# Performance work log

Hardware: AMD Instinct MI355X
Metric: run time of the kernel (lower is better)

## Reference

```python
import jax, jax.numpy as jnp
import numpy as np

H = 64          # hiddenNum
C3 = 3 * H      # 192 attention channels
FL = 7          # filterLen
PAD = FL // 2
NORM = 1.0 / np.sqrt(C3).astype(np.float32)


def _u(key, shape, stdv):
    return jax.random.uniform(key, shape, jnp.float32, -stdv, stdv)


def setup_inputs() -> dict:
    key = jax.random.key(0)
    ks = iter(jax.random.split(key, 64))
    B, N = 16, 1024
    x = jax.random.normal(next(ks), (B, N, 128), jnp.float32)
    adj = jax.random.uniform(next(ks), (B, N, N), jnp.float32)
    degree = jax.random.uniform(next(ks), (B, N, N), jnp.float32)
    eps = jax.random.normal(next(ks), (B, C3), jnp.float32) * 0.1
    d = {"x": x, "adj": adj, "degree": degree, "eps": eps}
    # GCN params (torch uniform(-1/sqrt(out), 1/sqrt(out)))
    for name, fi, fo in [("gcn1", 128, 2 * H), ("gcn2", H, 4 * H), ("gcn3", 2 * H, 6 * H)]:
        s = 1.0 / np.sqrt(fo)
        d[name + "_w"] = _u(next(ks), (fi, fo), s)
        d[name + "_b"] = _u(next(ks), (fo,), s)
    # Conv1d params [out, in, k]
    for name, ci, co in [("conv1", 128, 2 * H), ("conv2", H, 4 * H), ("conv3", 2 * H, 6 * H)]:
        s = 1.0 / np.sqrt(ci * FL)
        d[name + "_w"] = _u(next(ks), (co, ci, FL), s)
        d[name + "_b"] = _u(next(ks), (co,), s)
    # 1x1 conv Q/K/V projections
    s = 1.0 / np.sqrt(C3)
    for name in ["srq", "srk", "srv", "drq", "drk", "drv"]:
        d[name + "_w"] = _u(next(ks), (C3, C3, 1), s)
        d[name + "_b"] = _u(next(ks), (C3,), s)
    # Linear layers [out, in]
    for name in ["l1", "l2"]:
        d[name + "_w"] = _u(next(ks), (C3, C3), s)
        d[name + "_b"] = _u(next(ks), (C3,), s)
    return d


def _glu_last(y):
    o, g = jnp.split(y, 2, axis=-1)
    return o * jax.nn.sigmoid(g)


def _glu_ch(y):
    o, g = jnp.split(y, 2, axis=1)
    return o * jax.nn.sigmoid(g)


def _conv1d(x, w, b, pad):
    y = jax.lax.conv_general_dilated(x, w, (1,), [(pad, pad)],
                                     dimension_numbers=("NCH", "OIH", "NCH"))
    return y + b[None, :, None]


def reference(x, adj, degree, eps,
              gcn1_w, gcn1_b, gcn2_w, gcn2_b, gcn3_w, gcn3_b,
              conv1_w, conv1_b, conv2_w, conv2_b, conv3_w, conv3_b,
              srq_w, srq_b, srk_w, srk_b, srv_w, srv_b,
              drq_w, drq_b, drk_w, drk_b, drv_w, drv_b,
              l1_w, l1_b, l2_w, l2_b):
    # normalized adjacency: D @ A @ D  (batched dense bmm, as in the original)
    adj_n = jnp.matmul(jnp.matmul(degree, adj), degree)  # [B,N,N]

    def gcn(inp, W, b):
        return jnp.matmul(adj_n, inp @ W) + b

    # GCN branch with GLU gating (eval mode: dropout = identity)
    g1 = _glu_last(gcn(x, gcn1_w, gcn1_b))      # [B,N,H]
    g2 = _glu_last(gcn(g1, gcn2_w, gcn2_b))     # [B,N,2H]
    g3 = _glu_last(gcn(g2, gcn3_w, gcn3_b))     # [B,N,3H]
    gcn_out = jnp.transpose(g3, (0, 2, 1))      # [B,3H,N]

    # CNN branch with gated convs
    xc = jnp.transpose(x, (0, 2, 1))            # [B,128,N]
    c1 = _glu_ch(_conv1d(xc, conv1_w, conv1_b, PAD))   # [B,H,N]
    c2 = _glu_ch(_conv1d(c1, conv2_w, conv2_b, PAD))   # [B,2H,N]
    cnn_out = _glu_ch(_conv1d(c2, conv3_w, conv3_b, PAD))  # [B,3H,N]

    # 1x1-conv Q/K/V projections
    def p1x1(t, w, b):
        return jnp.einsum('oc,bcn->bon', w[:, :, 0], t) + b[None, :, None]

    SRQ = p1x1(cnn_out, srq_w, srq_b)
    SRK = p1x1(cnn_out, srk_w, srk_b)
    SRV = p1x1(cnn_out, srv_w, srv_b)
    DRQ = p1x1(gcn_out, drq_w, drq_b)
    DRK = p1x1(gcn_out, drk_w, drk_b)
    DRV = p1x1(gcn_out, drv_w, drv_b)

    # dual cross-attention; NOTE: scale applied AFTER softmax, as in the source
    attSR = jax.nn.softmax(jnp.einsum('bcn,bcm->bnm', SRQ, DRK), axis=-1) * NORM
    outSR = jnp.einsum('bnm,bcm->bnc', attSR, SRV)   # [B,N,3H]
    attDR = jax.nn.softmax(jnp.einsum('bcn,bcm->bnm', DRQ, SRK), axis=-1) * NORM
    outDR = jnp.einsum('bnm,bcm->bnc', attDR, DRV)   # [B,N,3H]

    feat = outSR + outDR                              # [B,N,3H]
    pooled = jnp.mean(feat, axis=1)                   # AdaptiveAvgPool1d(1) over N -> [B,3H]

    out1 = jax.nn.relu(pooled @ l1_w.T + l1_b)        # mean
    out2 = jax.nn.relu(pooled @ l2_w.T + l2_b)        # logvar
    std = jnp.exp(0.5 * out2)
    out0 = eps * std + out1                           # reparametrize
    return (out0, out1, out2)
```

## Files before the change

### kernel.cpp

```cpp
#include <hip/hip_runtime.h>


#define Bn 16
#define Nn 1024
#define C3n 192
static __device__ __constant__ float NORM_C = 0.07216878364870322f;

typedef short bf16x8 __attribute__((ext_vector_type(8)));
typedef float f32x4 __attribute__((ext_vector_type(4)));
typedef unsigned short u16;
typedef unsigned short u16x4 __attribute__((ext_vector_type(4)));

__device__ __forceinline__ u16 bf16rn(float x)
{
  unsigned b = __float_as_uint(x);
  b += 0x7fffu + ((b >> 16) & 1u);
  return (u16)(b >> 16);
}
__device__ __forceinline__ float fromh(u16 h) { return __uint_as_float(((unsigned)h) << 16); }

template<int TM, int TN, bool OUTB, int BIAS, bool ACC, bool OUTT>
__global__ __launch_bounds__(256, 2) void mgemm_k(
    const u16* __restrict__ A, long sA, int lda,
    const u16* __restrict__ B, long sB, int ldb,
    const float* __restrict__ bias,
    float* __restrict__ Cf, u16* __restrict__ Cb,
    int M, int N, int K)
{
  constexpr int WMN = (TM >= 128) ? 2 : 1;
  constexpr int WNN = 4 / WMN;
  constexpr int WTM = TM / WMN, WTN = TN / WNN;
  constexpr int FM = WTM / 16, FN = WTN / 16;
  constexpr int BBASE = TM * 128;
  __shared__ __align__(16) char sm[(TM + TN) * 128];

  const int bz = (int)blockIdx.z;
  const int n0 = blockIdx.x * TN, m0 = blockIdx.y * TM;
  const int tid = threadIdx.x, lane = tid & 63, w = tid >> 6;
  const int wm0 = (w / WNN) * WTM, wn0 = (w % WNN) * WTN;

  bf16x8 rA[TM / 32], rB[TN / 32];
  auto loadA = [&](int k0) {
    const u16* p = A + bz * sA + (long)m0 * lda + k0;
#pragma unroll
    for (int i = 0; i < TM / 32; ++i) {
      const int v = tid + i * 256, row = v >> 3, vc = v & 7;
      rA[i] = *(const bf16x8*)(p + (long)row * lda + vc * 8);
    }
  };
  auto storeA = [&]() {
#pragma unroll
    for (int i = 0; i < TM / 32; ++i) {
      const int v = tid + i * 256, row = v >> 3, vc = v & 7;
      *(bf16x8*)(sm + row * 128 + ((vc * 16) ^ ((row & 7) << 4))) = rA[i];
    }
  };
  auto loadB = [&](int k0) {
    const u16* p = B + bz * sB + (long)n0 * ldb + k0;
#pragma unroll
    for (int i = 0; i < TN / 32; ++i) {
      const int v = tid + i * 256, row = v >> 3, vc = v & 7;
      rB[i] = *(const bf16x8*)(p + (long)row * ldb + vc * 8);
    }
  };
  auto storeB = [&]() {
#pragma unroll
    for (int i = 0; i < TN / 32; ++i) {
      const int v = tid + i * 256, row = v >> 3, vc = v & 7;
      *(bf16x8*)(sm + BBASE + row * 128 + ((vc * 16) ^ ((row & 7) << 4))) = rB[i];
    }
  };

  f32x4 acc[FM][FN];
#pragma unroll
  for (int c = 0; c < FM; ++c)
#pragma unroll
    for (int d = 0; d < FN; ++d) acc[c][d] = (f32x4)(0.0f);

  loadA(0); loadB(0);
  for (int k0 = 0; k0 < K; k0 += 64) {
    storeA(); storeB();
    __syncthreads();
    if (k0 + 64 < K) { loadA(k0 + 64); loadB(k0 + 64); }
#pragma unroll
    for (int s = 0; s < 2; ++s) {
      const int kb = s * 64 + ((lane >> 4) << 4);
      bf16x8 ah[FM], bh[FN];
#pragma unroll
      for (int c = 0; c < FM; ++c) {
        const int ar = wm0 + c * 16 + (lane & 15);
        ah[c] = *(const bf16x8*)(sm + ar * 128 + (kb ^ ((ar & 7) << 4)));
      }
#pragma unroll
      for (int d = 0; d < FN; ++d) {
        const int br = wn0 + d * 16 + (lane & 15);
        bh[d] = *(const bf16x8*)(sm + BBASE + br * 128 + (kb ^ ((br & 7) << 4)));
      }
#pragma unroll
      for (int c = 0; c < FM; ++c)
#pragma unroll
        for (int d = 0; d < FN; ++d)
          acc[c][d] = __builtin_amdgcn_mfma_f32_16x16x32_bf16(ah[c], bh[d], acc[c][d], 0, 0, 0);
    }
    __syncthreads();
  }

  const long cb = (long)bz * M * N;
#pragma unroll
  for (int c = 0; c < FM; ++c)
#pragma unroll
    for (int d = 0; d < FN; ++d) {
      const int row0 = m0 + wm0 + c * 16 + (lane >> 4) * 4;
      const int col = n0 + wn0 + d * 16 + (lane & 15);
      if constexpr (OUTT) {
        u16x4 vv;
#pragma unroll
        for (int r = 0; r < 4; ++r) vv[r] = bf16rn(acc[c][d][r]);
        *(u16x4*)(Cb + cb + (long)col * M + row0) = vv;
      } else {
        float bcol = 0.f;
        if constexpr (BIAS == 1) bcol = bias[col];
#pragma unroll
        for (int r = 0; r < 4; ++r) {
          const int row = row0 + r;
          float v = acc[c][d][r];
          if constexpr (BIAS == 1) v += bcol;
          if constexpr (BIAS == 2) v += bias[row];
          const long idx = cb + (long)row * N + col;
          if constexpr (OUTB) {
            Cb[idx] = bf16rn(v);
          } else {
            if constexpr (ACC) v += Cf[idx];
            Cf[idx] = v;
          }
        }
      }
    }
}

__device__ __forceinline__ void gemm64_body(char* sm,
    const u16* __restrict__ A, int lda, const u16* __restrict__ B, int ldb,
    const float* __restrict__ bias, u16* __restrict__ Cb,
    int N, int K, int m0, int n0, bool biasRow)
{
  const int tid = threadIdx.x, lane = tid & 63, w = tid >> 6;
  bf16x8 rA[2], rB[2];
  auto loadA = [&](int k0) {
#pragma unroll
    for (int i = 0; i < 2; ++i) {
      const int v = tid + i * 256, row = v >> 3, vc = v & 7;
      rA[i] = *(const bf16x8*)(A + (long)(m0 + row) * lda + k0 + vc * 8);
    }
  };
  auto loadB = [&](int k0) {
#pragma unroll
    for (int i = 0; i < 2; ++i) {
      const int v = tid + i * 256, row = v >> 3, vc = v & 7;
      rB[i] = *(const bf16x8*)(B + (long)(n0 + row) * ldb + k0 + vc * 8);
    }
  };
  auto storeAB = [&]() {
#pragma unroll
    for (int i = 0; i < 2; ++i) {
      const int v = tid + i * 256, row = v >> 3, vc = v & 7;
      const int off = row * 128 + ((vc * 16) ^ ((row & 7) << 4));
      *(bf16x8*)(sm + off) = rA[i];
      *(bf16x8*)(sm + 8192 + off) = rB[i];
    }
  };

  f32x4 acc[4];
#pragma unroll
  for (int c = 0; c < 4; ++c) acc[c] = (f32x4)(0.0f);

  loadA(0); loadB(0);
  for (int k0 = 0; k0 < K; k0 += 64) {
    storeAB();
    __syncthreads();
    if (k0 + 64 < K) { loadA(k0 + 64); loadB(k0 + 64); }
#pragma unroll
    for (int s = 0; s < 2; ++s) {
      const int kb = s * 64 + ((lane >> 4) << 4);
      const int br = w * 16 + (lane & 15);
      const bf16x8 bh = *(const bf16x8*)(sm + 8192 + br * 128 + (kb ^ ((br & 7) << 4)));
#pragma unroll
      for (int c = 0; c < 4; ++c) {
        const int ar = c * 16 + (lane & 15);
        const bf16x8 ah = *(const bf16x8*)(sm + ar * 128 + (kb ^ ((ar & 7) << 4)));
        acc[c] = __builtin_amdgcn_mfma_f32_16x16x32_bf16(ah, bh, acc[c], 0, 0, 0);
      }
    }
    __syncthreads();
  }

  const int col = n0 + w * 16 + (lane & 15);
  const float bcol = biasRow ? 0.f : bias[col];
#pragma unroll
  for (int c = 0; c < 4; ++c) {
    const int row0 = m0 + c * 16 + (lane >> 4) * 4;
#pragma unroll
    for (int r = 0; r < 4; ++r) {
      const int row = row0 + r;
      const float bv = biasRow ? bias[row] : bcol;
      Cb[(long)row * N + col] = bf16rn(acc[c][r] + bv);
    }
  }
}

__global__ __launch_bounds__(256, 2) void qk4_k(
    const u16* __restrict__ inA, const u16* __restrict__ inB,
    const u16* __restrict__ w0, const u16* __restrict__ w1,
    const u16* __restrict__ w2, const u16* __restrict__ w3,
    const float* __restrict__ b0, const float* __restrict__ b1,
    const float* __restrict__ b2, const float* __restrict__ b3,
    u16* __restrict__ o0, u16* __restrict__ o1,
    u16* __restrict__ o2, u16* __restrict__ o3)
{
  __shared__ __align__(16) char sm[16384];
  constexpr long QS = (long)Nn * C3n;
  const int z = blockIdx.z, p = z >> 4, b = z & 15;
  const u16* in = (p < 2) ? inA : inB;
  const u16* W = (p == 0) ? w0 : (p == 1) ? w1 : (p == 2) ? w2 : w3;
  const float* bias = (p == 0) ? b0 : (p == 1) ? b1 : (p == 2) ? b2 : b3;
  u16* out = (p == 0) ? o0 : (p == 1) ? o1 : (p == 2) ? o2 : o3;
  gemm64_body(sm, in + (long)b * QS, C3n, W, C3n, bias, out + (long)b * QS,
              C3n, C3n, blockIdx.y * 64, blockIdx.x * 64, false);
}

__global__ __launch_bounds__(256, 2) void v2_k(
    const u16* __restrict__ inA, const u16* __restrict__ inB,
    const u16* __restrict__ w0, const u16* __restrict__ w1,
    const float* __restrict__ b0, const float* __restrict__ b1,
    u16* __restrict__ o0, u16* __restrict__ o1)
{
  __shared__ __align__(16) char sm[16384];
  constexpr long QS = (long)Nn * C3n;
  const int z = blockIdx.z, p = z >> 4, b = z & 15;
  const u16* in = p ? inB : inA;
  const u16* W = p ? w1 : w0;
  const float* bias = p ? b1 : b0;
  u16* out = p ? o1 : o0;
  gemm64_body(sm, W, C3n, in + (long)b * QS, C3n, bias, out + (long)b * QS,
              Nn, C3n, blockIdx.y * 64, blockIdx.x * 64, true);
}

template<int KC, bool OUTT>
__global__ __launch_bounds__(256, 2) void wglu_k(
    const u16* __restrict__ A, long sA,
    const u16* __restrict__ W,
    const float* __restrict__ bias,
    u16* __restrict__ G, long sG, int H)
{
  __shared__ __align__(16) char sm[3 * 8192];
  const int bz = blockIdx.z;
  const int h0 = blockIdx.x * 64, m0 = blockIdx.y * 64;
  const int tid = threadIdx.x, lane = tid & 63, w = tid >> 6;
  const int wn0 = w * 16;

  f32x4 accO[4], accG[4];
#pragma unroll
  for (int c = 0; c < 4; ++c) { accO[c] = (f32x4)(0.0f); accG[c] = (f32x4)(0.0f); }

  for (int k0 = 0; k0 < KC; k0 += 64) {
#pragma unroll
    for (int i = 0; i < 2; ++i) {
      const int v = tid + i * 256, row = v >> 3, vc = v & 7;
      const int off = row * 128 + ((vc * 16) ^ ((row & 7) << 4));
      *(bf16x8*)(sm + off) = *(const bf16x8*)(A + bz * sA + (long)(m0 + row) * KC + k0 + vc * 8);
      *(bf16x8*)(sm + 8192 + off) = *(const bf16x8*)(W + (long)(h0 + row) * KC + k0 + vc * 8);
      *(bf16x8*)(sm + 16384 + off) = *(const bf16x8*)(W + (long)(H + h0 + row) * KC + k0 + vc * 8);
    }
    __syncthreads();
#pragma unroll
    for (int s = 0; s < 2; ++s) {
      const int kb = s * 64 + ((lane >> 4) << 4);
      const int br = wn0 + (lane & 15);
      const bf16x8 bo = *(const bf16x8*)(sm + 8192 + br * 128 + (kb ^ ((br & 7) << 4)));
      const bf16x8 bg = *(const bf16x8*)(sm + 16384 + br * 128 + (kb ^ ((br & 7) << 4)));
#pragma unroll
      for (int c = 0; c < 4; ++c) {
        const int ar = c * 16 + (lane & 15);
        const bf16x8 a = *(const bf16x8*)(sm + ar * 128 + (kb ^ ((ar & 7) << 4)));
        accO[c] = __builtin_amdgcn_mfma_f32_16x16x32_bf16(a, bo, accO[c], 0, 0, 0);
        accG[c] = __builtin_amdgcn_mfma_f32_16x16x32_bf16(a, bg, accG[c], 0, 0, 0);
      }
    }
    __syncthreads();
  }

  const int col = h0 + wn0 + (lane & 15);
  const float bo = bias[col], bg = bias[H + col];
#pragma unroll
  for (int c = 0; c < 4; ++c) {
    const int row0 = m0 + c * 16 + (lane >> 4) * 4;
    if constexpr (OUTT) {
      u16x4 vv;
#pragma unroll
      for (int r = 0; r < 4; ++r) {
        const float o = accO[c][r] + bo, g = accG[c][r] + bg;
        vv[r] = bf16rn(o / (1.f + expf(-g)));
      }
      *(u16x4*)(G + bz * sG + (long)col * Nn + row0) = vv;
    } else {
#pragma unroll
      for (int r = 0; r < 4; ++r) {
        const float o = accO[c][r] + bo, g = accG[c][r] + bg;
        G[bz * sG + (long)(row0 + r) * H + col] = bf16rn(o / (1.f + expf(-g)));
      }
    }
  }
}

__global__ __launch_bounds__(256, 2) void conv_mfma_k(
    const u16* __restrict__ Wp, const u16* __restrict__ in_nm, int ldin, long sIn,
    u16* __restrict__ Z, long sZ, int Ci, int M)
{
  __shared__ __align__(16) char sm[9216 + 7 * 8192];
  const int bz = blockIdx.z;
  const int n0 = blockIdx.x * 64, m0 = blockIdx.y * 64;
  const int tid = threadIdx.x, lane = tid & 63, w = tid >> 6;
  const int wm = (w >> 1) * 32, wn = (w & 1) * 32;
  const u16* inb = in_nm + bz * sIn;

  f32x4 acc[2][2];
#pragma unroll
  for (int c = 0; c < 2; ++c)
#pragma unroll
    for (int d = 0; d < 2; ++d) acc[c][d] = (f32x4)(0.0f);

  for (int k0 = 0; k0 < Ci; k0 += 64) {
#pragma unroll
    for (int r = 0; r < 3; ++r) {
      const int idx = r * 256 + tid;
      if (idx < 576) {
        const int row = idx >> 3, ch = idx & 7;
        const int g = n0 + row - 3;
        bf16x8 v;
#pragma unroll
        for (int j = 0; j < 8; ++j) v[j] = 0;
        if ((unsigned)g < (unsigned)Nn)
          v = *(const bf16x8*)(inb + (long)g * ldin + k0 + ch * 8);
        *(bf16x8*)(sm + row * 128 + ((ch * 16) ^ ((row & 7) << 4))) = v;
      }
    }
#pragma unroll
    for (int i = 0; i < 14; ++i) {
      const int v = tid + i * 256;
      const int ft = v >> 9, rr = (v >> 3) & 63, vc = v & 7;
      const bf16x8 t = *(const bf16x8*)(Wp + ((long)ft * M + m0 + rr) * Ci + k0 + vc * 8);
      *(bf16x8*)(sm + 9216 + ft * 8192 + rr * 128 + ((vc * 16) ^ ((rr & 7) << 4))) = t;
    }
    __syncthreads();
#pragma unroll
    for (int ft = 0; ft < 7; ++ft) {
#pragma unroll
      for (int s = 0; s < 2; ++s) {
        const int kb = s * 64 + ((lane >> 4) << 4);
        bf16x8 ah[2], bh[2];
#pragma unroll
        for (int c = 0; c < 2; ++c) {
          const int ar = wm + c * 16 + (lane & 15);
          ah[c] = *(const bf16x8*)(sm + 9216 + ft * 8192 + ar * 128 + (kb ^ ((ar & 7) << 4)));
          const int hr = wn + c * 16 + (lane & 15) + ft;
          bh[c] = *(const bf16x8*)(sm + hr * 128 + (kb ^ ((hr & 7) << 4)));
        }
#pragma unroll
        for (int c = 0; c < 2; ++c)
#pragma unroll
          for (int d = 0; d < 2; ++d)
            acc[c][d] = __builtin_amdgcn_mfma_f32_16x16x32_bf16(ah[c], bh[d], acc[c][d], 0, 0, 0);
      }
    }
    __syncthreads();
  }

  u16* Zb = Z + bz * sZ;
#pragma unroll
  for (int c = 0; c < 2; ++c)
#pragma unroll
    for (int d = 0; d < 2; ++d) {
      const int row0 = m0 + wm + c * 16 + (lane >> 4) * 4;
      const int col = n0 + wn + d * 16 + (lane & 15);
#pragma unroll
      for (int r = 0; r < 4; ++r)
        Zb[(long)(row0 + r) * Nn + col] = bf16rn(acc[c][d][r]);
    }
}

__global__ __launch_bounds__(256, 2) void attn_k(
    const u16* __restrict__ Q0, const u16* __restrict__ K0,
    const u16* __restrict__ V0, float* __restrict__ O0,
    const u16* __restrict__ Q1, const u16* __restrict__ K1,
    const u16* __restrict__ V1, float* __restrict__ O1)
{
  constexpr long QS = (long)Nn * C3n;
  __shared__ __align__(16) char sm[81920];
  const int qb = blockIdx.x, b = blockIdx.y, at = blockIdx.z;
  const u16* Q = (at ? Q1 : Q0) + (long)b * QS + (long)qb * 64 * C3n;
  const u16* K = (at ? K1 : K0) + (long)b * QS;
  const u16* V = (at ? V1 : V0) + (long)b * QS;
  float* O = (at ? O1 : O0) + (long)b * QS;
  const int tid = threadIdx.x, lane = tid & 63, w = tid >> 6;

  bf16x8 vone;
#pragma unroll
  for (int j = 0; j < 8; ++j) vone[j] = (short)0x3F80;

  {
    const int row = tid >> 2;
#pragma unroll
    for (int j = 0; j < 6; ++j) {
      const int ch = (tid & 3) + j * 4;
      *(bf16x8*)(sm + row * 384 + ((ch * 16) ^ ((row & 7) << 4))) =
          *(const bf16x8*)(Q + (long)row * C3n + ch * 8);
    }
  }

  bf16x8 rK[6], rV[6];
  auto loadK = [&](int kb) {
    const int row = tid >> 2;
#pragma unroll
    for (int j = 0; j < 6; ++j) {
      const int ch = (tid & 3) + j * 4;
      rK[j] = *(const bf16x8*)(K + ((long)kb * 64 + row) * C3n + ch * 8);
    }
  };
  auto storeK = [&]() {
    const int row = tid >> 2;
#pragma unroll
    for (int j = 0; j < 6; ++j) {
      const int ch = (tid & 3) + j * 4;
      *(bf16x8*)(sm + 24576 + row * 384 + ((ch * 16) ^ ((row & 7) << 4))) = rK[j];
    }
  };
  auto loadV = [&](int kb) {
#pragma unroll
    for (int j = 0; j < 6; ++j) {
      const int row = (tid >> 3) + j * 32;
      const int ch = tid & 7;
      rV[j] = *(const bf16x8*)(V + (long)row * Nn + kb * 64 + ch * 8);
    }
  };
  auto storeV = [&]() {
#pragma unroll
    for (int j = 0; j < 6; ++j) {
      const int row = (tid >> 3) + j * 32;
      const int ch = tid & 7;
      *(bf16x8*)(sm + 49152 + row * 128 + ((ch * 16) ^ ((row & 7) << 4))) = rV[j];
    }
  };

  f32x4 accO[12], accL;
#pragma unroll
  for (int f = 0; f < 12; ++f) accO[f] = (f32x4)(0.0f);
  accL = (f32x4)(0.0f);
  float m[4];
#pragma unroll
  for (int r = 0; r < 4; ++r) m[r] = -3.0e38f;

  loadK(0);
  for (int kb = 0; kb < 16; ++kb) {
    storeK();
    __syncthreads();
    loadV(kb);

    f32x4 accS[4];
#pragma unroll
    for (int d = 0; d < 4; ++d) accS[d] = (f32x4)(0.0f);
    __builtin_amdgcn_s_setprio(1);
#pragma unroll
    for (int s = 0; s < 6; ++s) {
      const int kpos = s * 64 + ((lane >> 4) << 4);
      const int ar = w * 16 + (lane & 15);
      const bf16x8 a = *(const bf16x8*)(sm + ar * 384 + (kpos ^ ((ar & 7) << 4)));
#pragma unroll
      for (int d = 0; d < 4; ++d) {
        const int br = d * 16 + (lane & 15);
        const bf16x8 bb = *(const bf16x8*)(sm + 24576 + br * 384 + (kpos ^ ((br & 7) << 4)));
        accS[d] = __builtin_amdgcn_mfma_f32_16x16x32_bf16(a, bb, accS[d], 0, 0, 0);
      }
    }
    __builtin_amdgcn_s_setprio(0);

    float fac[4];
    bool need = false;
#pragma unroll
    for (int r = 0; r < 4; ++r) {
      float mx = fmaxf(fmaxf(accS[0][r], accS[1][r]), fmaxf(accS[2][r], accS[3][r]));
#pragma unroll
      for (int off = 8; off; off >>= 1) mx = fmaxf(mx, __shfl_xor(mx, off));
      float mn;
      if (mx > m[r] + 8.f) {
        mn = mx;
        fac[r] = __expf(m[r] - mn);
        m[r] = mn;
        need = true;
      } else {
        mn = m[r];
        fac[r] = 1.f;
      }
#pragma unroll
      for (int d = 0; d < 4; ++d) {
        float e = __expf(accS[d][r] - mn);
        if (e != e) e = (accS[d][r] == mn) ? 1.f : 0.f;
        accS[d][r] = e;
      }
    }
    if (__any(need)) {
#pragma unroll
      for (int f = 0; f < 12; ++f)
#pragma unroll
        for (int r = 0; r < 4; ++r) accO[f][r] *= fac[r];
#pragma unroll
      for (int r = 0; r < 4; ++r) accL[r] *= fac[r];
    }

    {
      const int qbase = w * 16 + (lane >> 4) * 4;
#pragma unroll
      for (int r = 0; r < 4; ++r) {
        const int qr = qbase + r;
#pragma unroll
        for (int d = 0; d < 4; ++d) {
          const int colb = (d * 16 + (lane & 15)) * 2;
          *(u16*)(sm + 73728 + qr * 128 + (colb ^ ((qr & 7) << 4))) = bf16rn(accS[d][r]);
        }
      }
    }
    storeV();
    __syncthreads();
    if (kb < 15) loadK(kb + 1);

    __builtin_amdgcn_s_setprio(1);
#pragma unroll
    for (int s = 0; s < 2; ++s) {
      const int kpos = s * 64 + ((lane >> 4) << 4);
      const int ar = w * 16 + (lane & 15);
      const bf16x8 a = *(const bf16x8*)(sm + 73728 + ar * 128 + (kpos ^ ((ar & 7) << 4)));
#pragma unroll
      for (int f = 0; f < 12; ++f) {
        const int br = f * 16 + (lane & 15);
        const bf16x8 bb = *(const bf16x8*)(sm + 49152 + br * 128 + (kpos ^ ((br & 7) << 4)));
        accO[f] = __builtin_amdgcn_mfma_f32_16x16x32_bf16(a, bb, accO[f], 0, 0, 0);
      }
      accL = __builtin_amdgcn_mfma_f32_16x16x32_bf16(a, vone, accL, 0, 0, 0);
    }
    __builtin_amdgcn_s_setprio(0);
  }

#pragma unroll
  for (int r = 0; r < 4; ++r) {
    const int row = qb * 64 + w * 16 + (lane >> 4) * 4 + r;
    const float inv = NORM_C / accL[r];
#pragma unroll
    for (int f = 0; f < 12; ++f)
      O[(long)row * C3n + f * 16 + (lane & 15)] = accO[f][r] * inv;
  }
}

__global__ void cvt2_k(const float* __restrict__ a, const float* __restrict__ b,
                       u16* __restrict__ da, u16* __restrict__ db, long half4)
{
  const long i = (long)blockIdx.x * 256 + threadIdx.x;
  if (i >= 2 * half4) return;
  const bool second = (i >= half4);
  const long j = second ? i - half4 : i;
  float4 v = ((const float4*)(second ? b : a))[j];
  u16x4 o = {bf16rn(v.x), bf16rn(v.y), bf16rn(v.z), bf16rn(v.w)};
  ((u16x4*)(second ? db : da))[j] = o;
}

__global__ void xcvt2_k(const float* __restrict__ x, u16* __restrict__ xh,
                        u16* __restrict__ xc)
{
  __shared__ float t[32][33];
  const int b = blockIdx.z;
  const int n0 = blockIdx.x * 32, c0 = blockIdx.y * 32;
  const int tx = threadIdx.x, ty = threadIdx.y;
#pragma unroll
  for (int i = 0; i < 32; i += 8) {
    const float v = x[((long)b * Nn + n0 + ty + i) * 128 + c0 + tx];
    t[ty + i][tx] = v;
    xh[((long)b * Nn + n0 + ty + i) * 128 + c0 + tx] = bf16rn(v);
  }
  __syncthreads();
#pragma unroll
  for (int i = 0; i < 32; i += 8)
    xc[((long)b * 128 + c0 + ty + i) * Nn + n0 + tx] = bf16rn(t[tx][ty + i]);
}

__global__ void cvtw6_k(const float* s0, const float* s1, const float* s2,
                        const float* s3, const float* s4, const float* s5,
                        u16* d0, u16* d1, u16* d2, u16* d3, u16* d4, u16* d5)
{
  const int which = blockIdx.y;
  const float* s = which==0?s0:which==1?s1:which==2?s2:which==3?s3:which==4?s4:s5;
  u16* d = which==0?d0:which==1?d1:which==2?d2:which==3?d3:which==4?d4:d5;
  const int i = blockIdx.x * 256 + threadIdx.x;
  if (i >= 192*192/4) return;
  float4 v = ((const float4*)s)[i];
  u16x4 o = {bf16rn(v.x), bf16rn(v.y), bf16rn(v.z), bf16rn(v.w)};
  ((u16x4*)d)[i] = o;
}

__global__ void wt_k(const float* __restrict__ W, u16* __restrict__ Wt, int R, int C)
{
  __shared__ float t[32][33];
  const int c0 = blockIdx.x * 32, r0 = blockIdx.y * 32;
  const int tx = threadIdx.x, ty = threadIdx.y;
#pragma unroll
  for (int i = 0; i < 32; i += 8)
    t[ty + i][tx] = W[(long)(r0 + ty + i) * C + c0 + tx];
  __syncthreads();
#pragma unroll
  for (int i = 0; i < 32; i += 8)
    Wt[(long)(c0 + ty + i) * R + r0 + tx] = bf16rn(t[tx][ty + i]);
}

__global__ void wp_k(const float* __restrict__ w, u16* __restrict__ Wp, int Co, int Ci)
{
  const int idx = blockIdx.x * 256 + threadIdx.x;
  if (idx >= Co * Ci * 7) return;
  const int ft = idx / (Co * Ci);
  const int rem = idx - ft * Co * Ci;
  const int co = rem / Ci, ci = rem - co * Ci;
  Wp[idx] = bf16rn(w[((long)co * Ci + ci) * 7 + ft]);
}

__global__ void glu_cht_k(const u16* __restrict__ Z, const float* __restrict__ bias,
                          u16* __restrict__ G, int H)
{
  __shared__ float t[32][33];
  const int b = blockIdx.z;
  const int n0 = blockIdx.x * 32, h0 = blockIdx.y * 32;
  const int tx = threadIdx.x, ty = threadIdx.y;
  const u16* Zb = Z + (long)b * 2 * H * Nn;
#pragma unroll
  for (int i = 0; i < 32; i += 8) {
    const int h = h0 + ty + i;
    const float o = fromh(Zb[(long)h * Nn + n0 + tx]) + bias[h];
    const float g = fromh(Zb[(long)(H + h) * Nn + n0 + tx]) + bias[H + h];
    t[ty + i][tx] = o / (1.f + expf(-g));
  }
  __syncthreads();
#pragma unroll
  for (int i = 0; i < 32; i += 8)
    G[((long)b * Nn + n0 + ty + i) * H + h0 + tx] = bf16rn(t[tx][ty + i]);
}

__global__ void pool_k(const float* __restrict__ fa, const float* __restrict__ fb,
                       float* __restrict__ ppart)
{
  const int chunk = blockIdx.x, b = blockIdx.y;
  const int c = threadIdx.x;
  const long base = ((long)b * Nn + chunk * 128) * C3n + c;
  float s = 0.f;
  for (int n = 0; n < 128; ++n) s += fa[base + (long)n * C3n] + fb[base + (long)n * C3n];
  ppart[(b * 8 + chunk) * C3n + c] = s;
}

__device__ __forceinline__ float sanitize(float v)
{
  if (v != v) return 0.f;
  return fminf(fmaxf(v, -3.0e38f), 3.0e38f);
}

__global__ void head_k(const float* __restrict__ ppart,
                       const float* __restrict__ l1w, const float* __restrict__ l1b,
                       const float* __restrict__ l2w, const float* __restrict__ l2b,
                       const float* __restrict__ eps, float* __restrict__ out)
{
  const int b = blockIdx.x, o = threadIdx.x;
  __shared__ float sp[C3n];
  float sacc = 0.f;
  for (int k = 0; k < 8; ++k) sacc += ppart[(b * 8 + k) * C3n + o];
  sp[o] = sacc * (1.f / Nn);
  __syncthreads();
  float d1 = l1b[o], d2 = l2b[o];
  for (int c = 0; c < C3n; ++c) {
    d1 = fmaf(sp[c], l1w[o * C3n + c], d1);
    d2 = fmaf(sp[c], l2w[o * C3n + c], d2);
  }
  const float o1 = fmaxf(d1, 0.f);
  const float o2 = fmaxf(d2, 0.f);
  const float sd = fminf(expf(0.5f * o2), 3.0e38f);
  const double v0 = (double)eps[b * C3n + o] * (double)sd + (double)o1;
  out[b * C3n + o] = sanitize((float)fmin(fmax(v0, -3.0e38), 3.0e38));
  out[Bn * C3n + b * C3n + o] = sanitize(o1);
  out[2 * Bn * C3n + b * C3n + o] = sanitize(o2);
}

extern "C" void kernel_launch(void* const* d_in, const int* in_sizes, int n_in,
                              void* d_out, int out_size, void* d_ws, size_t ws_size,
                              hipStream_t stream)
{
  const float* x    = (const float*)d_in[0];
  const float* adjm = (const float*)d_in[1];
  const float* deg  = (const float*)d_in[2];
  const float* eps  = (const float*)d_in[3];
  const float* g1w  = (const float*)d_in[4];
  const float* g1b  = (const float*)d_in[5];
  const float* g2w  = (const float*)d_in[6];
  const float* g2b  = (const float*)d_in[7];
  const float* g3w  = (const float*)d_in[8];
  const float* g3b  = (const float*)d_in[9];
  const float* c1w  = (const float*)d_in[10];
  const float* c1b  = (const float*)d_in[11];
  const float* c2w  = (const float*)d_in[12];
  const float* c2b  = (const float*)d_in[13];
  const float* c3w  = (const float*)d_in[14];
  const float* c3b  = (const float*)d_in[15];
  const float* srqw = (const float*)d_in[16];
  const float* srqb = (const float*)d_in[17];
  const float* srkw = (const float*)d_in[18];
  const float* srkb = (const float*)d_in[19];
  const float* srvw = (const float*)d_in[20];
  const float* srvb = (const float*)d_in[21];
  const float* drqw = (const float*)d_in[22];
  const float* drqb = (const float*)d_in[23];
  const float* drkw = (const float*)d_in[24];
  const float* drkb = (const float*)d_in[25];
  const float* drvw = (const float*)d_in[26];
  const float* drvb = (const float*)d_in[27];
  const float* l1w  = (const float*)d_in[28];
  const float* l1b  = (const float*)d_in[29];
  const float* l2w  = (const float*)d_in[30];
  const float* l2b  = (const float*)d_in[31];
  float* out = (float*)d_out;
  char* ws = (char*)d_ws;

  constexpr long MBc = 1L << 20;
  u16*  DEGB = (u16*)(ws + 0*MBc);
  u16*  ADJB = (u16*)(ws + 34*MBc);
  u16*  Z    = (u16*)(ws + 68*MBc);
  u16*  c1b16= (u16*)(ws + 94*MBc);
  u16*  c2b16= (u16*)(ws + 97*MBc);
  u16*  T1   = (u16*)(ws + 94*MBc);
  u16*  T2   = (u16*)(ws + 99*MBc);
  u16*  Pb   = (u16*)(ws + 104*MBc);
  u16*  CNN  = (u16*)(ws + 109*MBc);
  u16*  G3   = (u16*)(ws + 116*MBc);
  u16*  xh   = (u16*)(ws + 123*MBc);
  u16*  xch  = (u16*)(ws + 128*MBc);
  u16*  G1   = (u16*)(ws + 133*MBc);
  u16*  G2   = (u16*)(ws + 136*MBc);
  u16*  SRQ = (u16*)(ws + 0*MBc);
  u16*  SRK = (u16*)(ws + 7*MBc);
  u16*  DRQ = (u16*)(ws + 14*MBc);
  u16*  DRK = (u16*)(ws + 21*MBc);
  u16*  SRV = (u16*)(ws + 28*MBc);
  u16*  DRV = (u16*)(ws + 35*MBc);
  float* FEATA = (float*)(ws + 43*MBc);
  float* FEATB = (float*)(ws + 57*MBc);

  long wb = 141 * MBc;
  auto aU = [&](long elems) { u16* p = (u16*)(ws + wb); wb += elems * 2; wb = (wb + 255) & ~255L; return p; };
  u16* W1t = aU(128*128);
  u16* W2t = aU(256*64);
  u16* W3t = aU(384*128);
  u16* WP1 = aU(7*128*128);
  u16* WP2 = aU(7*256*64);
  u16* WP3 = aU(7*384*128);
  u16* QW[6];
  for (int i = 0; i < 6; ++i) QW[i] = aU(192*192);
  float* PPART = (float*)(ws + wb);

  const long sNN = (long)Nn * Nn;
  const long QS = (long)Nn * C3n;
  const long sCM128 = (long)128 * Nn;

  cvt2_k<<<32768, 256, 0, stream>>>(deg, adjm, DEGB, ADJB, sNN * Bn / 4);
  xcvt2_k<<<dim3(32,4,Bn), dim3(32,8), 0, stream>>>(x, xh, xch);
  wt_k<<<dim3(4,4), dim3(32,8), 0, stream>>>(g1w, W1t, 128, 128);
  wt_k<<<dim3(8,2), dim3(32,8), 0, stream>>>(g2w, W2t, 64, 256);
  wt_k<<<dim3(12,4), dim3(32,8), 0, stream>>>(g3w, W3t, 128, 384);
  wp_k<<<(128*128*7+255)/256, 256, 0, stream>>>(c1w, WP1, 128, 128);
  wp_k<<<(256*64*7+255)/256, 256, 0, stream>>>(c2w, WP2, 256, 64);
  wp_k<<<(384*128*7+255)/256, 256, 0, stream>>>(c3w, WP3, 384, 128);
  cvtw6_k<<<dim3(36, 6), 256, 0, stream>>>(srqw, srkw, srvw, drqw, drkw, drvw,
                                           QW[0], QW[1], QW[2], QW[3], QW[4], QW[5]);

  conv_mfma_k<<<dim3(16,2,Bn), 256, 0, stream>>>(WP1, xh, 128, (long)Nn*128, Z, sCM128, 128, 128);
  glu_cht_k<<<dim3(32,2,Bn), dim3(32,8), 0, stream>>>(Z, c1b, c1b16, 64);
  conv_mfma_k<<<dim3(16,4,Bn), 256, 0, stream>>>(WP2, c1b16, 64, (long)Nn*64, Z, (long)256*Nn, 64, 256);
  glu_cht_k<<<dim3(32,4,Bn), dim3(32,8), 0, stream>>>(Z, c2b, c2b16, 128);
  conv_mfma_k<<<dim3(16,6,Bn), 256, 0, stream>>>(WP3, c2b16, 128, (long)Nn*128, Z, (long)384*Nn, 128, 384);
  glu_cht_k<<<dim3(32,6,Bn), dim3(32,8), 0, stream>>>(Z, c3b, CNN, 192);

  mgemm_k<64,64,false,0,false,true><<<dim3(2,16,Bn), 256, 0, stream>>>(
      DEGB, sNN, Nn, xch, sCM128, Nn, nullptr, nullptr, T1, Nn, 128, Nn);
  mgemm_k<64,64,false,0,false,true><<<dim3(2,16,Bn), 256, 0, stream>>>(
      ADJB, sNN, Nn, T1, sCM128, Nn, nullptr, nullptr, T2, Nn, 128, Nn);
  mgemm_k<64,64,true,0,false,false><<<dim3(2,16,Bn), 256, 0, stream>>>(
      DEGB, sNN, Nn, T2, sCM128, Nn, nullptr, nullptr, Pb, Nn, 128, Nn);
  wglu_k<128,true><<<dim3(1,16,Bn), 256, 0, stream>>>(
      Pb, (long)Nn*128, W1t, g1b, G1, (long)64*Nn, 64);
  mgemm_k<64,64,false,0,false,true><<<dim3(1,16,Bn), 256, 0, stream>>>(
      DEGB, sNN, Nn, G1, (long)64*Nn, Nn, nullptr, nullptr, T1, Nn, 64, Nn);
  mgemm_k<64,64,false,0,false,true><<<dim3(1,16,Bn), 256, 0, stream>>>(
      ADJB, sNN, Nn, T1, (long)64*Nn, Nn, nullptr, nullptr, T2, Nn, 64, Nn);
  mgemm_k<64,64,true,0,false,false><<<dim3(1,16,Bn), 256, 0, stream>>>(
      DEGB, sNN, Nn, T2, (long)64*Nn, Nn, nullptr, nullptr, Pb, Nn, 64, Nn);
  wglu_k<64,true><<<dim3(2,16,Bn), 256, 0, stream>>>(
      Pb, (long)Nn*64, W2t, g2b, G2, sCM128, 128);
  mgemm_k<64,64,false,0,false,true><<<dim3(2,16,Bn), 256, 0, stream>>>(
      DEGB, sNN, Nn, G2, sCM128, Nn, nullptr, nullptr, T1, Nn, 128, Nn);
  mgemm_k<64,64,false,0,false,true><<<dim3(2,16,Bn), 256, 0, stream>>>(
      ADJB, sNN, Nn, T1, sCM128, Nn, nullptr, nullptr, T2, Nn, 128, Nn);
  mgemm_k<64,64,true,0,false,false><<<dim3(2,16,Bn), 256, 0, stream>>>(
      DEGB, sNN, Nn, T2, sCM128, Nn, nullptr, nullptr, Pb, Nn, 128, Nn);
  wglu_k<128,false><<<dim3(3,16,Bn), 256, 0, stream>>>(
      Pb, (long)Nn*128, W3t, g3b, G3, QS, 192);

  qk4_k<<<dim3(3,16,64), 256, 0, stream>>>(
      CNN, G3, QW[0], QW[1], QW[3], QW[4], srqb, srkb, drqb, drkb,
      SRQ, SRK, DRQ, DRK);
  v2_k<<<dim3(16,3,32), 256, 0, stream>>>(
      CNN, G3, QW[2], QW[5], srvb, drvb, SRV, DRV);

  attn_k<<<dim3(16, Bn, 2), 256, 0, stream>>>(
      SRQ, DRK, SRV, FEATA, DRQ, SRK, DRV, FEATB);

  pool_k<<<dim3(8, Bn), C3n, 0, stream>>>(FEATA, FEATB, PPART);
  head_k<<<Bn, C3n, 0, stream>>>(PPART, l1w, l1b, l2w, l2b, eps, out);
}
```

Baseline: 348.4 us.

## Fuse mean-pooling into attention epilogue and merge weight-prep kernels

The attention kernel no longer writes the full [B,N,3H] fp32 outputs. It reduces its 64 query rows per block in registers, with shuffles and shared memory, into per-block partial column sums, and the head kernel sums those partials. This removes the pool kernel and the large feature write and read-back. Separately, the conv-weight permute and Q/K/V weight conversion launches are merged into one kernel, trading vectorized float4 conversion for scalar work to cut launch count.

```diff
diff --git a/kernel.cpp b/kernel.cpp
--- a/kernel.cpp
+++ b/kernel.cpp
@@ -389,9 +389,10 @@
 
 __global__ __launch_bounds__(256, 2) void attn_k(
     const u16* __restrict__ Q0, const u16* __restrict__ K0,
-    const u16* __restrict__ V0, float* __restrict__ O0,
+    const u16* __restrict__ V0,
     const u16* __restrict__ Q1, const u16* __restrict__ K1,
-    const u16* __restrict__ V1, float* __restrict__ O1)
+    const u16* __restrict__ V1,
+    float* __restrict__ PSUM)
 {
   constexpr long QS = (long)Nn * C3n;
   __shared__ __align__(16) char sm[81920];
@@ -399,7 +400,6 @@
   const u16* Q = (at ? Q1 : Q0) + (long)b * QS + (long)qb * 64 * C3n;
   const u16* K = (at ? K1 : K0) + (long)b * QS;
   const u16* V = (at ? V1 : V0) + (long)b * QS;
-  float* O = (at ? O1 : O0) + (long)b * QS;
   const int tid = threadIdx.x, lane = tid & 63, w = tid >> 6;
 
   bf16x8 vone;
@@ -548,13 +548,27 @@
     __builtin_amdgcn_s_setprio(0);
   }
 
-#pragma unroll
-  for (int r = 0; r < 4; ++r) {
-    const int row = qb * 64 + w * 16 + (lane >> 4) * 4 + r;
-    const float inv = NORM_C / accL[r];
-#pragma unroll
-    for (int f = 0; f < 12; ++f)
-      O[(long)row * C3n + f * 16 + (lane & 15)] = accO[f][r] * inv;
+  float inv[4];
+#pragma unroll
+  for (int r = 0; r < 4; ++r) inv[r] = NORM_C / accL[r];
+  float s[12];
+#pragma unroll
+  for (int f = 0; f < 12; ++f) {
+    s[f] = accO[f][0] * inv[0] + accO[f][1] * inv[1]
+         + accO[f][2] * inv[2] + accO[f][3] * inv[3];
+    s[f] += __shfl_xor(s[f], 16);
+    s[f] += __shfl_xor(s[f], 32);
+  }
+  __syncthreads();
+  float* red = (float*)sm;
+  if ((lane >> 4) == 0) {
+#pragma unroll
+    for (int f = 0; f < 12; ++f) red[w * 192 + f * 16 + (lane & 15)] = s[f];
+  }
+  __syncthreads();
+  if (tid < 192) {
+    const float t = red[tid] + red[192 + tid] + red[384 + tid] + red[576 + tid];
+    PSUM[(((long)at * 16 + b) * 16 + qb) * 192 + tid] = t;
   }
 }
 
@@ -589,18 +603,32 @@
     xc[((long)b * 128 + c0 + ty + i) * Nn + n0 + tx] = bf16rn(t[tx][ty + i]);
 }
 
-__global__ void cvtw6_k(const float* s0, const float* s1, const float* s2,
-                        const float* s3, const float* s4, const float* s5,
-                        u16* d0, u16* d1, u16* d2, u16* d3, u16* d4, u16* d5)
-{
-  const int which = blockIdx.y;
-  const float* s = which==0?s0:which==1?s1:which==2?s2:which==3?s3:which==4?s4:s5;
-  u16* d = which==0?d0:which==1?d1:which==2?d2:which==3?d3:which==4?d4:d5;
-  const int i = blockIdx.x * 256 + threadIdx.x;
-  if (i >= 192*192/4) return;
-  float4 v = ((const float4*)s)[i];
-  u16x4 o = {bf16rn(v.x), bf16rn(v.y), bf16rn(v.z), bf16rn(v.w)};
-  ((u16x4*)d)[i] = o;
+__global__ void prep9_k(
+    const float* c1w, const float* c2w, const float* c3w,
+    u16* wp1, u16* wp2, u16* wp3,
+    const float* q0, const float* q1, const float* q2,
+    const float* q3, const float* q4, const float* q5,
+    u16* d0, u16* d1, u16* d2, u16* d3, u16* d4, u16* d5)
+{
+  const int job = blockIdx.y;
+  const int idx = blockIdx.x * 256 + threadIdx.x;
+  if (job < 3) {
+    const float* w = job == 0 ? c1w : job == 1 ? c2w : c3w;
+    u16* Wp = job == 0 ? wp1 : job == 1 ? wp2 : wp3;
+    const int Co = job == 0 ? 128 : job == 1 ? 256 : 384;
+    const int Ci = job == 1 ? 64 : 128;
+    if (idx >= Co * Ci * 7) return;
+    const int ft = idx / (Co * Ci);
+    const int rem = idx - ft * Co * Ci;
+    const int co = rem / Ci, ci = rem - co * Ci;
+    Wp[idx] = bf16rn(w[((long)co * Ci + ci) * 7 + ft]);
+  } else {
+    const int q = job - 3;
+    const float* s = q==0?q0:q==1?q1:q==2?q2:q==3?q3:q==4?q4:q5;
+    u16* d = q==0?d0:q==1?d1:q==2?d2:q==3?d3:q==4?d4:d5;
+    if (idx >= 192 * 192) return;
+    d[idx] = bf16rn(s[idx]);
+  }
 }
 
 __global__ void wt_k(const float* __restrict__ W, u16* __restrict__ Wt, int R, int C)
@@ -615,16 +643,6 @@
 #pragma unroll
   for (int i = 0; i < 32; i += 8)
     Wt[(long)(c0 + ty + i) * R + r0 + tx] = bf16rn(t[tx][ty + i]);
-}
-
-__global__ void wp_k(const float* __restrict__ w, u16* __restrict__ Wp, int Co, int Ci)
-{
-  const int idx = blockIdx.x * 256 + threadIdx.x;
-  if (idx >= Co * Ci * 7) return;
-  const int ft = idx / (Co * Ci);
-  const int rem = idx - ft * Co * Ci;
-  const int co = rem / Ci, ci = rem - co * Ci;
-  Wp[idx] = bf16rn(w[((long)co * Ci + ci) * 7 + ft]);
 }
 
 __global__ void glu_cht_k(const u16* __restrict__ Z, const float* __restrict__ bias,
@@ -648,24 +666,13 @@
     G[((long)b * Nn + n0 + ty + i) * H + h0 + tx] = bf16rn(t[tx][ty + i]);
 }
 
-__global__ void pool_k(const float* __restrict__ fa, const float* __restrict__ fb,
-                       float* __restrict__ ppart)
-{
-  const int chunk = blockIdx.x, b = blockIdx.y;
-  const int c = threadIdx.x;
-  const long base = ((long)b * Nn + chunk * 128) * C3n + c;
-  float s = 0.f;
-  for (int n = 0; n < 128; ++n) s += fa[base + (long)n * C3n] + fb[base + (long)n * C3n];
-  ppart[(b * 8 + chunk) * C3n + c] = s;
-}
-
 __device__ __forceinline__ float sanitize(float v)
 {
   if (v != v) return 0.f;
   return fminf(fmaxf(v, -3.0e38f), 3.0e38f);
 }
 
-__global__ void head_k(const float* __restrict__ ppart,
+__global__ void head_k(const float* __restrict__ psum,
                        const float* __restrict__ l1w, const float* __restrict__ l1b,
                        const float* __restrict__ l2w, const float* __restrict__ l2b,
                        const float* __restrict__ eps, float* __restrict__ out)
@@ -673,7 +680,10 @@
   const int b = blockIdx.x, o = threadIdx.x;
   __shared__ float sp[C3n];
   float sacc = 0.f;
-  for (int k = 0; k < 8; ++k) sacc += ppart[(b * 8 + k) * C3n + o];
+#pragma unroll
+  for (int at = 0; at < 2; ++at)
+    for (int q = 0; q < 16; ++q)
+      sacc += psum[(((long)at * 16 + b) * 16 + q) * 192 + o];
   sp[o] = sacc * (1.f / Nn);
   __syncthreads();
   float d1 = l1b[o], d2 = l2b[o];
@@ -750,8 +760,7 @@
   u16*  DRK = (u16*)(ws + 21*MBc);
   u16*  SRV = (u16*)(ws + 28*MBc);
   u16*  DRV = (u16*)(ws + 35*MBc);
-  float* FEATA = (float*)(ws + 43*MBc);
-  float* FEATB = (float*)(ws + 57*MBc);
+  float* PSUM = (float*)(ws + 43*MBc);
 
   long wb = 141 * MBc;
   auto aU = [&](long elems) { u16* p = (u16*)(ws + wb); wb += elems * 2; wb = (wb + 255) & ~255L; return p; };
@@ -763,7 +772,6 @@
   u16* WP3 = aU(7*384*128);
   u16* QW[6];
   for (int i = 0; i < 6; ++i) QW[i] = aU(192*192);
-  float* PPART = (float*)(ws + wb);
 
   const long sNN = (long)Nn * Nn;
   const long QS = (long)Nn * C3n;
@@ -774,11 +782,10 @@
   wt_k<<<dim3(4,4), dim3(32,8), 0, stream>>>(g1w, W1t, 128, 128);
   wt_k<<<dim3(8,2), dim3(32,8), 0, stream>>>(g2w, W2t, 64, 256);
   wt_k<<<dim3(12,4), dim3(32,8), 0, stream>>>(g3w, W3t, 128, 384);
-  wp_k<<<(128*128*7+255)/256, 256, 0, stream>>>(c1w, WP1, 128, 128);
-  wp_k<<<(256*64*7+255)/256, 256, 0, stream>>>(c2w, WP2, 256, 64);
-  wp_k<<<(384*128*7+255)/256, 256, 0, stream>>>(c3w, WP3, 384, 128);
-  cvtw6_k<<<dim3(36, 6), 256, 0, stream>>>(srqw, srkw, srvw, drqw, drkw, drvw,
-                                           QW[0], QW[1], QW[2], QW[3], QW[4], QW[5]);
+  prep9_k<<<dim3(1344, 9), 256, 0, stream>>>(
+      c1w, c2w, c3w, WP1, WP2, WP3,
+      srqw, srkw, srvw, drqw, drkw, drvw,
+      QW[0], QW[1], QW[2], QW[3], QW[4], QW[5]);
 
   conv_mfma_k<<<dim3(16,2,Bn), 256, 0, stream>>>(WP1, xh, 128, (long)Nn*128, Z, sCM128, 128, 128);
   glu_cht_k<<<dim3(32,2,Bn), dim3(32,8), 0, stream>>>(Z, c1b, c1b16, 64);
@@ -819,8 +826,7 @@
       CNN, G3, QW[2], QW[5], srvb, drvb, SRV, DRV);
 
   attn_k<<<dim3(16, Bn, 2), 256, 0, stream>>>(
-      SRQ, DRK, SRV, FEATA, DRQ, SRK, DRV, FEATB);
-
-  pool_k<<<dim3(8, Bn), C3n, 0, stream>>>(FEATA, FEATB, PPART);
-  head_k<<<Bn, C3n, 0, stream>>>(PPART, l1w, l1b, l2w, l2b, eps, out);
-}
+      SRQ, DRK, SRV, DRQ, SRK, DRV, PSUM);
+
+  head_k<<<Bn, C3n, 0, stream>>>(PSUM, l1w, l1b, l2w, l2b, eps, out);
+}
```

After: 335.7 us. 3.7% less time.
